# Kernel optimization log

Hardware: AMD Instinct MI355X
Metric: run time of the kernel (lower is better)

The kernel has to match this reference:

```python
import jax, jax.numpy as jnp
import numpy as np

N, E, D, L = 100000, 600000, 128, 5
BN_EPS = 1e-5


def setup_inputs() -> dict:
    key = jax.random.key(0)
    ks = jax.random.split(key, 12)
    x = jax.random.normal(ks[0], (N, D), dtype=jnp.float32)
    edge_index = jax.random.randint(ks[1], (2, E), 0, N, dtype=jnp.int64)
    edge_attr = jax.random.randint(ks[2], (E, D), 0, 4, dtype=jnp.int32)
    # per-layer GCNConv params
    W = jax.random.normal(ks[3], (L, D, D), dtype=jnp.float32) * 0.05
    b = jax.random.normal(ks[4], (L, D), dtype=jnp.float32) * 0.01
    root = jax.random.normal(ks[5], (L, D), dtype=jnp.float32) * 0.05
    # BatchNorm1d eval-mode params / running stats
    gamma = 1.0 + 0.1 * jax.random.normal(ks[6], (L, D), dtype=jnp.float32)
    beta = 0.1 * jax.random.normal(ks[7], (L, D), dtype=jnp.float32)
    mean = 0.1 * jax.random.normal(ks[8], (L, D), dtype=jnp.float32)
    var = 0.5 + jax.random.uniform(ks[9], (L, D), dtype=jnp.float32)
    return {"x": x, "edge_index": edge_index, "edge_attr": edge_attr,
            "W": W, "b": b, "root": root,
            "gamma": gamma, "beta": beta, "mean": mean, "var": var}


def reference(x, edge_index, edge_attr, W, b, root, gamma, beta, mean, var):
    # edge_attr.long() then identity edge_encoder -> integer values used in float math
    e = edge_attr.astype(x.dtype)                      # [E, D]
    row, col = edge_index[0], edge_index[1]            # source j, target i
    # deg = degree(row) + 1 (same every layer since graph is fixed)
    deg = jax.ops.segment_sum(jnp.ones((E,), x.dtype), row, num_segments=N) + 1.0  # [N]
    dinv = deg ** -0.5
    norm = (dinv[row] * dinv[col])[:, None]            # [E, 1]
    h = x
    for l in range(L):
        hl = h @ W[l].T + b[l]                         # Linear(emb_dim, emb_dim)
        msg = norm * jax.nn.relu(hl[row] + e)          # gather + relu + scale  [E, D]
        agg = jax.ops.segment_sum(msg, col, num_segments=N)  # scatter-add at targets
        h = agg + jax.nn.relu(hl + root[l]) / deg[:, None]   # self-loop term
        # BatchNorm1d (eval mode, running stats)
        h = gamma[l] * (h - mean[l]) / jnp.sqrt(var[l] + BN_EPS) + beta[l]
        if l < L - 1:
            h = jax.nn.relu(h)                         # dropout is identity in eval
    return h  # JK='last'
```

## Files before the change

kernel.cpp:

```cpp
#include <hip/hip_runtime.h>
#include <cstdint>
#include <cstddef>

#define DF 128
#define NL 5
#define BN_EPS 1e-5f

typedef short bf16x8 __attribute__((ext_vector_type(8)));
typedef float f32x4 __attribute__((ext_vector_type(4)));

typedef __attribute__((address_space(3))) uint32_t lds_u32;
typedef __attribute__((address_space(1))) uint32_t glb_u32;

__device__ __forceinline__ void gload16(const void* g, void* l) {
#if __has_builtin(__builtin_amdgcn_global_load_lds)
  __builtin_amdgcn_global_load_lds((const glb_u32*)g, (lds_u32*)l, 16, 0, 0);
#else
  *(uint4*)l = *(const uint4*)g;
#endif
}

__device__ __forceinline__ ushort f2b(float f) {
  union { float f; uint32_t u; } v; v.f = f;
  uint32_t u = v.u + 0x7fffu + ((v.u >> 16) & 1u);
  return (ushort)(u >> 16);
}
__device__ __forceinline__ float b2f(uint32_t lo16) {
  union { uint32_t u; float f; } v; v.u = lo16 << 16;
  return v.f;
}
__device__ __forceinline__ uint32_t pk2(float a, float b) {
  return (uint32_t)f2b(a) | ((uint32_t)f2b(b) << 16);
}


__global__ void k_deg2(const int* __restrict__ row, const int* __restrict__ col,
                       int* __restrict__ degi, int* __restrict__ indeg, int E) {
  int i = blockIdx.x * blockDim.x + threadIdx.x;
  if (i < E) {
    atomicAdd(&degi[row[i]], 1);
    atomicAdd(&indeg[col[i]], 1);
  }
}

__global__ void k_dinv(const int* __restrict__ degi, float* __restrict__ dinv, int N) {
  int i = blockIdx.x * blockDim.x + threadIdx.x;
  if (i < N) dinv[i] = 1.0f / sqrtf((float)(degi[i] + 1));
}

__global__ void k_start(const int* __restrict__ indeg, int* __restrict__ start,
                        int* __restrict__ cursor, int* __restrict__ counter, int N) {
  int i = blockIdx.x * blockDim.x + threadIdx.x;
  if (i < N) {
    int s = atomicAdd(counter, indeg[i]);
    start[i] = s;
    cursor[i] = s;
  }
}

__global__ void k_fillpack(const int* __restrict__ row, const int* __restrict__ col,
                           const float* __restrict__ dinv, int* __restrict__ cursor,
                           int* __restrict__ srcS, float* __restrict__ nrmS,
                           const int* __restrict__ ea, uint32_t* __restrict__ epS, int E) {
  int tid = blockIdx.x * blockDim.x + threadIdx.x;
  int e = tid >> 3, t = tid & 7;
  if (e >= E) return;
  int pos;
  if (t == 0) {
    int r = row[e], c = col[e];
    pos = atomicAdd(&cursor[c], 1);
    srcS[pos] = r;
    nrmS[pos] = dinv[r] * dinv[c];
  }
  pos = __shfl(pos, 0, 8);
  const int4* p = ((const int4*)ea) + (size_t)e * 32 + t * 4;
  uint32_t w = 0;
  #pragma unroll
  for (int q = 0; q < 4; ++q) {
    int4 a = p[q];
    w |= ((uint32_t)(a.x & 3)) << (8 * q);
    w |= ((uint32_t)(a.y & 3)) << (8 * q + 2);
    w |= ((uint32_t)(a.z & 3)) << (8 * q + 4);
    w |= ((uint32_t)(a.w & 3)) << (8 * q + 6);
  }
  epS[(size_t)pos * 8 + t] = w;
}

__global__ void k_params(const float* __restrict__ g, const float* __restrict__ be,
                         const float* __restrict__ mn, const float* __restrict__ vr,
                         float* __restrict__ s, float* __restrict__ t,
                         const float* __restrict__ W, ushort* __restrict__ Wb,
                         int nbn, int nw) {
  int i = blockIdx.x * blockDim.x + threadIdx.x;
  if (i < nw) Wb[i] = f2b(W[i]);
  if (i < nbn) {
    float sc = g[i] / sqrtf(vr[i] + BN_EPS);
    s[i] = sc;
    t[i] = be[i] - mn[i] * sc;
  }
}

template <typename IT, typename AT>
__global__ __launch_bounds__(256) void k_gemm(
    const IT* in, const ushort* __restrict__ Wb,
    const float* __restrict__ bl, const float* __restrict__ rootl,
    const float* __restrict__ sl, const float* __restrict__ tl,
    const float* __restrict__ dinv,
    ushort* __restrict__ hl, AT* accOut, int N)
{
  __shared__ uint4 lA[128 * 16];
  __shared__ uint4 lW[128 * 16];
  const int t = threadIdx.x;
  const int row0 = blockIdx.x * 128;
  const int wv = t >> 6;
  const int l  = t & 63;

  #pragma unroll
  for (int it = 0; it < 8; ++it) {
    int ubase = (it * 4 + wv) * 64;
    int lin = ubase + l;
    int r = lin >> 4, u = lin & 15;
    gload16((const uint4*)Wb + (r << 4) + (u ^ (r & 7)), lA  + 0 == nullptr ? nullptr : (void*)(lW + ubase));
  }

  if constexpr (sizeof(IT) == 2) {
    #pragma unroll
    for (int it = 0; it < 8; ++it) {
      int ubase = (it * 4 + wv) * 64;
      int lin = ubase + l;
      int r = lin >> 4, u = lin & 15;
      int gn = row0 + r;
      int gnc = gn < N ? gn : N - 1;
      gload16((const uint4*)in + (size_t)gnc * 16 + (u ^ (r & 7)), (void*)(lA + ubase));
    }
  } else {
    #pragma unroll
    for (int it = 0; it < 8; ++it) {
      int lin = it * 256 + t;
      int r = lin >> 4, u = lin & 15;
      int gn = row0 + r;
      uint4 pk = make_uint4(0u, 0u, 0u, 0u);
      if (gn < N) {
        const float4* p = (const float4*)((const float*)in + (size_t)gn * DF + u * 8);
        float4 f0 = p[0], f1 = p[1];
        pk.x = pk2(f0.x, f0.y); pk.y = pk2(f0.z, f0.w);
        pk.z = pk2(f1.x, f1.y); pk.w = pk2(f1.z, f1.w);
      }
      lA[(r << 4) | (u ^ (r & 7))] = pk;
    }
  }
  __syncthreads();

  const int lr = l & 15;
  const int lk = l >> 4;

  f32x4 acc[2][8];
  #pragma unroll
  for (int rt = 0; rt < 2; ++rt)
    #pragma unroll
    for (int ct = 0; ct < 8; ++ct) acc[rt][ct] = (f32x4){0.f, 0.f, 0.f, 0.f};

  #pragma unroll
  for (int ks = 0; ks < 4; ++ks) {
    const int kofs = ks * 4 + lk;
    bf16x8 af[2], wf[8];
    #pragma unroll
    for (int rt = 0; rt < 2; ++rt) {
      int r = wv * 32 + rt * 16 + lr;
      af[rt] = *reinterpret_cast<const bf16x8*>(&lA[(r << 4) | (kofs ^ (r & 7))]);
    }
    #pragma unroll
    for (int ct = 0; ct < 8; ++ct) {
      int r = ct * 16 + lr;
      wf[ct] = *reinterpret_cast<const bf16x8*>(&lW[(r << 4) | (kofs ^ (r & 7))]);
    }
    #pragma unroll
    for (int rt = 0; rt < 2; ++rt)
      #pragma unroll
      for (int ct = 0; ct < 8; ++ct)
        acc[rt][ct] = __builtin_amdgcn_mfma_f32_16x16x32_bf16(af[rt], wf[ct], acc[rt][ct], 0, 0, 0);
  }

  float bb[8], rr[8], ss[8], tt[8];
  #pragma unroll
  for (int ct = 0; ct < 8; ++ct) {
    int c = ct * 16 + lr;
    bb[ct] = bl[c]; rr[ct] = rootl[c]; ss[ct] = sl[c]; tt[ct] = tl[c];
  }

  #pragma unroll
  for (int rt = 0; rt < 2; ++rt) {
    #pragma unroll
    for (int rg = 0; rg < 4; ++rg) {
      int gn = row0 + wv * 32 + rt * 16 + lk * 4 + rg;
      if (gn >= N) continue;
      float di = dinv[gn];
      float invdeg = di * di;
      #pragma unroll
      for (int ct = 0; ct < 8; ++ct) {
        int c = ct * 16 + lr;
        float o = acc[rt][ct][rg] + bb[ct];
        hl[(size_t)gn * DF + c] = f2b(o);
        float se = fmaxf(o + rr[ct], 0.f) * invdeg;
        float av2 = ss[ct] * se + tt[ct];
        if constexpr (sizeof(AT) == 4) accOut[(size_t)gn * DF + c] = av2;
        else                           accOut[(size_t)gn * DF + c] = f2b(av2);
      }
    }
  }
}

template <typename AT, bool RELU>
__global__ __launch_bounds__(256) void k_gather(
    const int* __restrict__ start, const int* __restrict__ indeg,
    const int* __restrict__ srcS, const float* __restrict__ nrmS,
    const uint32_t* __restrict__ epS,
    const uint4* __restrict__ hl4,
    const float* __restrict__ sl,
    AT* acc, int N)
{
  int gw = (blockIdx.x * blockDim.x + threadIdx.x) >> 6;
  int lane = threadIdx.x & 63;
  int s16 = lane & 15;
  int nd = gw * 4 + (lane >> 4);
  if (nd >= N) return;
  int base = start[nd], n = indeg[nd];
  const uint32_t sh = (s16 & 1) * 16;
  const int dw = s16 >> 1;

  float a[8];
  #pragma unroll
  for (int j = 0; j < 8; ++j) a[j] = 0.f;

  for (int c0 = 0; c0 < n; c0 += 16) {
    int m = min(16, n - c0);
    int myIdx = base + c0 + s16;
    int mySrc = (s16 < m) ? srcS[myIdx] : 0;
    float myNrm = (s16 < m) ? nrmS[myIdx] : 0.f;
    #pragma unroll 2
    for (int k = 0; k < m; ++k) {
      int src = __shfl(mySrc, k, 16);
      float nr = __shfl(myNrm, k, 16);
      uint32_t pw = epS[(size_t)(base + c0 + k) * 8 + dw];
      uint4 hw = hl4[(size_t)src * 16 + s16];
      float h, ev;
      h = b2f(hw.x & 0xffffu); ev = (float)((pw >> (sh + 0)) & 3u);  a[0] += nr * fmaxf(h + ev, 0.f);
      h = b2f(hw.x >> 16);     ev = (float)((pw >> (sh + 2)) & 3u);  a[1] += nr * fmaxf(h + ev, 0.f);
      h = b2f(hw.y & 0xffffu); ev = (float)((pw >> (sh + 4)) & 3u);  a[2] += nr * fmaxf(h + ev, 0.f);
      h = b2f(hw.y >> 16);     ev = (float)((pw >> (sh + 6)) & 3u);  a[3] += nr * fmaxf(h + ev, 0.f);
      h = b2f(hw.z & 0xffffu); ev = (float)((pw >> (sh + 8)) & 3u);  a[4] += nr * fmaxf(h + ev, 0.f);
      h = b2f(hw.z >> 16);     ev = (float)((pw >> (sh + 10)) & 3u); a[5] += nr * fmaxf(h + ev, 0.f);
      h = b2f(hw.w & 0xffffu); ev = (float)((pw >> (sh + 12)) & 3u); a[6] += nr * fmaxf(h + ev, 0.f);
      h = b2f(hw.w >> 16);     ev = (float)((pw >> (sh + 14)) & 3u); a[7] += nr * fmaxf(h + ev, 0.f);
    }
  }

  float s8[8];
  ((float4*)s8)[0] = ((const float4*)sl)[s16 * 2];
  ((float4*)s8)[1] = ((const float4*)sl)[s16 * 2 + 1];

  if constexpr (sizeof(AT) == 2) {
    uint4* ap = (uint4*)acc + (size_t)nd * 16 + s16;
    uint4 p = *ap;
    float o[8];
    o[0] = b2f(p.x & 0xffffu) + s8[0] * a[0];
    o[1] = b2f(p.x >> 16)     + s8[1] * a[1];
    o[2] = b2f(p.y & 0xffffu) + s8[2] * a[2];
    o[3] = b2f(p.y >> 16)     + s8[3] * a[3];
    o[4] = b2f(p.z & 0xffffu) + s8[4] * a[4];
    o[5] = b2f(p.z >> 16)     + s8[5] * a[5];
    o[6] = b2f(p.w & 0xffffu) + s8[6] * a[6];
    o[7] = b2f(p.w >> 16)     + s8[7] * a[7];
    if (RELU) {
      #pragma unroll
      for (int j = 0; j < 8; ++j) o[j] = fmaxf(o[j], 0.f);
    }
    p.x = pk2(o[0], o[1]); p.y = pk2(o[2], o[3]);
    p.z = pk2(o[4], o[5]); p.w = pk2(o[6], o[7]);
    *ap = p;
  } else {
    float4* ap = (float4*)acc + (size_t)nd * 32 + s16 * 2;
    float4 p0 = ap[0], p1 = ap[1];
    p0.x += s8[0] * a[0]; p0.y += s8[1] * a[1];
    p0.z += s8[2] * a[2]; p0.w += s8[3] * a[3];
    p1.x += s8[4] * a[4]; p1.y += s8[5] * a[5];
    p1.z += s8[6] * a[6]; p1.w += s8[7] * a[7];
    if (RELU) {
      p0.x = fmaxf(p0.x, 0.f); p0.y = fmaxf(p0.y, 0.f);
      p0.z = fmaxf(p0.z, 0.f); p0.w = fmaxf(p0.w, 0.f);
      p1.x = fmaxf(p1.x, 0.f); p1.y = fmaxf(p1.y, 0.f);
      p1.z = fmaxf(p1.z, 0.f); p1.w = fmaxf(p1.w, 0.f);
    }
    ap[0] = p0; ap[1] = p1;
  }
}

extern "C" void kernel_launch(void* const* d_in, const int* in_sizes, int n_in,
                              void* d_out, int out_size, void* d_ws, size_t ws_size,
                              hipStream_t stream) {
  const float* x     = (const float*)d_in[0];
  const int*   ei    = (const int*)d_in[1];
  const int*   ea    = (const int*)d_in[2];
  const float* W     = (const float*)d_in[3];
  const float* b     = (const float*)d_in[4];
  const float* root  = (const float*)d_in[5];
  const float* gamma = (const float*)d_in[6];
  const float* beta  = (const float*)d_in[7];
  const float* mean  = (const float*)d_in[8];
  const float* var   = (const float*)d_in[9];

  const int N = in_sizes[0] / DF;
  const int E = in_sizes[1] / 2;
  const int* row = ei;
  const int* col = ei + E;

  char* ws = (char*)d_ws;
  size_t off = 0;
  auto alloc = [&](size_t bytes) -> void* {
    void* p = ws + off;
    off = (off + bytes + 255) & ~(size_t)255;
    return p;
  };
  int*      degi   = (int*)alloc((size_t)N * 4);
  int*      indeg  = (int*)alloc((size_t)N * 4);
  int*      counter= (int*)alloc(256);
  size_t    zspan  = (size_t)((char*)ws + off - (char*)degi);
  float*    dinv   = (float*)alloc((size_t)N * 4);
  int*      startA = (int*)alloc((size_t)N * 4);
  int*      cursor = (int*)alloc((size_t)N * 4);
  int*      srcS   = (int*)alloc((size_t)E * 4);
  float*    nrmS   = (float*)alloc((size_t)E * 4);
  uint32_t* epS    = (uint32_t*)alloc((size_t)E * 8 * 4);
  float*    sbuf   = (float*)alloc((size_t)NL * DF * 4);
  float*    tbuf   = (float*)alloc((size_t)NL * DF * 4);
  ushort*   Wb     = (ushort*)alloc((size_t)NL * DF * DF * 2);
  ushort*   hl     = (ushort*)alloc((size_t)N * DF * 2);
  ushort*   accA   = (ushort*)alloc((size_t)N * DF * 2);

  hipMemsetAsync(degi, 0, zspan, stream);

  k_deg2<<<(E + 255) / 256, 256, 0, stream>>>(row, col, degi, indeg, E);
  k_dinv<<<(N + 255) / 256, 256, 0, stream>>>(degi, dinv, N);
  k_start<<<(N + 255) / 256, 256, 0, stream>>>(indeg, startA, cursor, counter, N);
  k_fillpack<<<(E * 8 + 255) / 256, 256, 0, stream>>>(row, col, dinv, cursor,
                                                      srcS, nrmS, ea, epS, E);
  k_params<<<(NL * DF * DF + 255) / 256, 256, 0, stream>>>(
      gamma, beta, mean, var, sbuf, tbuf, W, Wb, NL * DF, NL * DF * DF);

  float* outp = (float*)d_out;
  const int gemmGrid = (N + 127) / 128;
  const int gathGrid = ((N + 3) / 4 * 64 + 255) / 256;

  k_gemm<float, ushort><<<gemmGrid, 256, 0, stream>>>(
      x, Wb, b, root, sbuf, tbuf, dinv, hl, accA, N);
  k_gather<ushort, true><<<gathGrid, 256, 0, stream>>>(
      startA, indeg, srcS, nrmS, epS, (const uint4*)hl, sbuf, accA, N);

  for (int l = 1; l < NL - 1; ++l) {
    k_gemm<ushort, ushort><<<gemmGrid, 256, 0, stream>>>(
        accA, Wb + (size_t)l * DF * DF, b + (size_t)l * DF, root + (size_t)l * DF,
        sbuf + (size_t)l * DF, tbuf + (size_t)l * DF, dinv, hl, accA, N);
    k_gather<ushort, true><<<gathGrid, 256, 0, stream>>>(
        startA, indeg, srcS, nrmS, epS, (const uint4*)hl,
        sbuf + (size_t)l * DF, accA, N);
  }

  {
    const int l = NL - 1;
    k_gemm<ushort, float><<<gemmGrid, 256, 0, stream>>>(
        accA, Wb + (size_t)l * DF * DF, b + (size_t)l * DF, root + (size_t)l * DF,
        sbuf + (size_t)l * DF, tbuf + (size_t)l * DF, dinv, hl, outp, N);
    k_gather<float, false><<<gathGrid, 256, 0, stream>>>(
        startA, indeg, srcS, nrmS, epS, (const uint4*)hl,
        sbuf + (size_t)l * DF, outp, N);
  }
}
```

Baseline: 464.3 us.

## Renumber nodes by in-degree buckets and move self-loop epilogue into gather

```diff
diff --git a/kernel.cpp b/kernel.cpp
--- a/kernel.cpp
+++ b/kernel.cpp
@@ -4,6 +4,7 @@
 
 #define DF 128
 #define NL 5
+#define NB 1024
 #define BN_EPS 1e-5f
 
 typedef short bf16x8 __attribute__((ext_vector_type(8)));
@@ -43,23 +44,58 @@
   }
 }
 
-__global__ void k_dinv(const int* __restrict__ degi, float* __restrict__ dinv, int N) {
-  int i = blockIdx.x * blockDim.x + threadIdx.x;
-  if (i < N) dinv[i] = 1.0f / sqrtf((float)(degi[i] + 1));
-}
-
-__global__ void k_start(const int* __restrict__ indeg, int* __restrict__ start,
-                        int* __restrict__ cursor, int* __restrict__ counter, int N) {
+__global__ void k_dinvhist(const int* __restrict__ degi, const int* __restrict__ indeg,
+                           float* __restrict__ dinv, int* __restrict__ hist, int N) {
   int i = blockIdx.x * blockDim.x + threadIdx.x;
   if (i < N) {
-    int s = atomicAdd(counter, indeg[i]);
-    start[i] = s;
-    cursor[i] = s;
-  }
+    dinv[i] = 1.0f / sqrtf((float)(degi[i] + 1));
+    atomicAdd(&hist[min(indeg[i], NB - 1)], 1);
+  }
+}
+
+__global__ void k_scan(const int* __restrict__ hist,
+                       int* __restrict__ nodeStart, int* __restrict__ edgeStart) {
+  __shared__ int2 sm[NB];
+  int t = threadIdx.x;
+  int c = hist[t];
+  int2 v; v.x = c; v.y = c * t;
+  sm[t] = v;
+  __syncthreads();
+  for (int off = 1; off < NB; off <<= 1) {
+    int2 add; add.x = 0; add.y = 0;
+    if (t >= off) add = sm[t - off];
+    __syncthreads();
+    sm[t].x += add.x; sm[t].y += add.y;
+    __syncthreads();
+  }
+  nodeStart[t] = sm[t].x - c;
+  edgeStart[t] = sm[t].y - c * t;
+}
+
+__global__ void k_assign(const int* __restrict__ indeg, const float* __restrict__ dinv,
+                         const int* __restrict__ nodeStart, const int* __restrict__ edgeStart,
+                         int* __restrict__ binCursor,
+                         int* __restrict__ perm, int* __restrict__ invperm,
+                         int* __restrict__ startP, int* __restrict__ cursorP,
+                         int* __restrict__ degP, float* __restrict__ dinvP, int N) {
+  int nd = blockIdx.x * blockDim.x + threadIdx.x;
+  if (nd >= N) return;
+  int d = indeg[nd];
+  int bin = min(d, NB - 1);
+  int r = atomicAdd(&binCursor[bin], 1);
+  int i = nodeStart[bin] + r;
+  perm[i] = nd;
+  invperm[nd] = i;
+  int st = edgeStart[bin] + r * d;
+  startP[i] = st;
+  cursorP[i] = st;
+  degP[i] = d;
+  dinvP[i] = dinv[nd];
 }
 
 __global__ void k_fillpack(const int* __restrict__ row, const int* __restrict__ col,
-                           const float* __restrict__ dinv, int* __restrict__ cursor,
+                           const float* __restrict__ dinv, const int* __restrict__ invperm,
+                           int* __restrict__ cursorP,
                            int* __restrict__ srcS, float* __restrict__ nrmS,
                            const int* __restrict__ ea, uint32_t* __restrict__ epS, int E) {
   int tid = blockIdx.x * blockDim.x + threadIdx.x;
@@ -68,8 +104,8 @@
   int pos;
   if (t == 0) {
     int r = row[e], c = col[e];
-    pos = atomicAdd(&cursor[c], 1);
-    srcS[pos] = r;
+    pos = atomicAdd(&cursorP[invperm[c]], 1);
+    srcS[pos] = invperm[r];
     nrmS[pos] = dinv[r] * dinv[c];
   }
   pos = __shfl(pos, 0, 8);
@@ -100,13 +136,11 @@
   }
 }
 
-template <typename IT, typename AT>
+template <typename IT>
 __global__ __launch_bounds__(256) void k_gemm(
-    const IT* in, const ushort* __restrict__ Wb,
-    const float* __restrict__ bl, const float* __restrict__ rootl,
-    const float* __restrict__ sl, const float* __restrict__ tl,
-    const float* __restrict__ dinv,
-    ushort* __restrict__ hl, AT* accOut, int N)
+    const IT* __restrict__ in, const int* __restrict__ perm,
+    const ushort* __restrict__ Wb, const float* __restrict__ bl,
+    ushort* __restrict__ hl, int N)
 {
   __shared__ uint4 lA[128 * 16];
   __shared__ uint4 lW[128 * 16];
@@ -120,7 +154,7 @@
     int ubase = (it * 4 + wv) * 64;
     int lin = ubase + l;
     int r = lin >> 4, u = lin & 15;
-    gload16((const uint4*)Wb + (r << 4) + (u ^ (r & 7)), lA  + 0 == nullptr ? nullptr : (void*)(lW + ubase));
+    gload16((const void*)((const uint4*)Wb + (r << 4) + (u ^ (r & 7))), (void*)(lW + ubase));
   }
 
   if constexpr (sizeof(IT) == 2) {
@@ -131,7 +165,8 @@
       int r = lin >> 4, u = lin & 15;
       int gn = row0 + r;
       int gnc = gn < N ? gn : N - 1;
-      gload16((const uint4*)in + (size_t)gnc * 16 + (u ^ (r & 7)), (void*)(lA + ubase));
+      gload16((const void*)((const uint4*)in + (size_t)gnc * 16 + (u ^ (r & 7))),
+              (void*)(lA + ubase));
     }
   } else {
     #pragma unroll
@@ -141,7 +176,8 @@
       int gn = row0 + r;
       uint4 pk = make_uint4(0u, 0u, 0u, 0u);
       if (gn < N) {
-        const float4* p = (const float4*)((const float*)in + (size_t)gn * DF + u * 8);
+        int src = perm[gn];
+        const float4* p = (const float4*)((const float*)in + (size_t)src * DF + u * 8);
         float4 f0 = p[0], f1 = p[1];
         pk.x = pk2(f0.x, f0.y); pk.y = pk2(f0.z, f0.w);
         pk.z = pk2(f1.x, f1.y); pk.w = pk2(f1.z, f1.w);
@@ -181,12 +217,9 @@
         acc[rt][ct] = __builtin_amdgcn_mfma_f32_16x16x32_bf16(af[rt], wf[ct], acc[rt][ct], 0, 0, 0);
   }
 
-  float bb[8], rr[8], ss[8], tt[8];
-  #pragma unroll
-  for (int ct = 0; ct < 8; ++ct) {
-    int c = ct * 16 + lr;
-    bb[ct] = bl[c]; rr[ct] = rootl[c]; ss[ct] = sl[c]; tt[ct] = tl[c];
-  }
+  float bb[8];
+  #pragma unroll
+  for (int ct = 0; ct < 8; ++ct) bb[ct] = bl[ct * 16 + lr];
 
   #pragma unroll
   for (int rt = 0; rt < 2; ++rt) {
@@ -194,37 +227,32 @@
     for (int rg = 0; rg < 4; ++rg) {
       int gn = row0 + wv * 32 + rt * 16 + lk * 4 + rg;
       if (gn >= N) continue;
-      float di = dinv[gn];
-      float invdeg = di * di;
       #pragma unroll
-      for (int ct = 0; ct < 8; ++ct) {
-        int c = ct * 16 + lr;
-        float o = acc[rt][ct][rg] + bb[ct];
-        hl[(size_t)gn * DF + c] = f2b(o);
-        float se = fmaxf(o + rr[ct], 0.f) * invdeg;
-        float av2 = ss[ct] * se + tt[ct];
-        if constexpr (sizeof(AT) == 4) accOut[(size_t)gn * DF + c] = av2;
-        else                           accOut[(size_t)gn * DF + c] = f2b(av2);
-      }
-    }
-  }
-}
-
-template <typename AT, bool RELU>
+      for (int ct = 0; ct < 8; ++ct)
+        hl[(size_t)gn * DF + ct * 16 + lr] = f2b(acc[rt][ct][rg] + bb[ct]);
+    }
+  }
+}
+
+template <typename AT, bool LAST>
 __global__ __launch_bounds__(256) void k_gather(
-    const int* __restrict__ start, const int* __restrict__ indeg,
+    const int* __restrict__ startP, const int* __restrict__ degP,
+    const float* __restrict__ dinvP,
     const int* __restrict__ srcS, const float* __restrict__ nrmS,
     const uint32_t* __restrict__ epS,
     const uint4* __restrict__ hl4,
-    const float* __restrict__ sl,
-    AT* acc, int N)
+    const float* __restrict__ rootl, const float* __restrict__ sl,
+    const float* __restrict__ tl, const int* __restrict__ perm,
+    AT* __restrict__ acc, int N)
 {
   int gw = (blockIdx.x * blockDim.x + threadIdx.x) >> 6;
   int lane = threadIdx.x & 63;
   int s16 = lane & 15;
-  int nd = gw * 4 + (lane >> 4);
-  if (nd >= N) return;
-  int base = start[nd], n = indeg[nd];
+  int i = gw * 4 + (lane >> 4);
+  if (i >= N) return;
+  int base = startP[i], n = degP[i];
+  float di = dinvP[i];
+  float invdeg = di * di;
   const uint32_t sh = (s16 & 1) * 16;
   const int dw = s16 >> 1;
 
@@ -255,43 +283,37 @@
     }
   }
 
-  float s8[8];
-  ((float4*)s8)[0] = ((const float4*)sl)[s16 * 2];
-  ((float4*)s8)[1] = ((const float4*)sl)[s16 * 2 + 1];
-
-  if constexpr (sizeof(AT) == 2) {
-    uint4* ap = (uint4*)acc + (size_t)nd * 16 + s16;
-    uint4 p = *ap;
-    float o[8];
-    o[0] = b2f(p.x & 0xffffu) + s8[0] * a[0];
-    o[1] = b2f(p.x >> 16)     + s8[1] * a[1];
-    o[2] = b2f(p.y & 0xffffu) + s8[2] * a[2];
-    o[3] = b2f(p.y >> 16)     + s8[3] * a[3];
-    o[4] = b2f(p.z & 0xffffu) + s8[4] * a[4];
-    o[5] = b2f(p.z >> 16)     + s8[5] * a[5];
-    o[6] = b2f(p.w & 0xffffu) + s8[6] * a[6];
-    o[7] = b2f(p.w >> 16)     + s8[7] * a[7];
-    if (RELU) {
-      #pragma unroll
-      for (int j = 0; j < 8; ++j) o[j] = fmaxf(o[j], 0.f);
-    }
+  uint4 hwS = hl4[(size_t)i * 16 + s16];
+  float hs[8];
+  hs[0] = b2f(hwS.x & 0xffffu); hs[1] = b2f(hwS.x >> 16);
+  hs[2] = b2f(hwS.y & 0xffffu); hs[3] = b2f(hwS.y >> 16);
+  hs[4] = b2f(hwS.z & 0xffffu); hs[5] = b2f(hwS.z >> 16);
+  hs[6] = b2f(hwS.w & 0xffffu); hs[7] = b2f(hwS.w >> 16);
+
+  float rr[8], ss[8], tt[8];
+  ((float4*)rr)[0] = ((const float4*)rootl)[s16 * 2]; ((float4*)rr)[1] = ((const float4*)rootl)[s16 * 2 + 1];
+  ((float4*)ss)[0] = ((const float4*)sl)[s16 * 2];    ((float4*)ss)[1] = ((const float4*)sl)[s16 * 2 + 1];
+  ((float4*)tt)[0] = ((const float4*)tl)[s16 * 2];    ((float4*)tt)[1] = ((const float4*)tl)[s16 * 2 + 1];
+
+  float o[8];
+  #pragma unroll
+  for (int j = 0; j < 8; ++j) {
+    float self = fmaxf(hs[j] + rr[j], 0.f) * invdeg;
+    o[j] = ss[j] * (self + a[j]) + tt[j];
+  }
+
+  if constexpr (!LAST) {
+    #pragma unroll
+    for (int j = 0; j < 8; ++j) o[j] = fmaxf(o[j], 0.f);
+    uint4 p;
     p.x = pk2(o[0], o[1]); p.y = pk2(o[2], o[3]);
     p.z = pk2(o[4], o[5]); p.w = pk2(o[6], o[7]);
-    *ap = p;
+    ((uint4*)acc)[(size_t)i * 16 + s16] = p;
   } else {
+    int nd = perm[i];
     float4* ap = (float4*)acc + (size_t)nd * 32 + s16 * 2;
-    float4 p0 = ap[0], p1 = ap[1];
-    p0.x += s8[0] * a[0]; p0.y += s8[1] * a[1];
-    p0.z += s8[2] * a[2]; p0.w += s8[3] * a[3];
-    p1.x += s8[4] * a[4]; p1.y += s8[5] * a[5];
-    p1.z += s8[6] * a[6]; p1.w += s8[7] * a[7];
-    if (RELU) {
-      p0.x = fmaxf(p0.x, 0.f); p0.y = fmaxf(p0.y, 0.f);
-      p0.z = fmaxf(p0.z, 0.f); p0.w = fmaxf(p0.w, 0.f);
-      p1.x = fmaxf(p1.x, 0.f); p1.y = fmaxf(p1.y, 0.f);
-      p1.z = fmaxf(p1.z, 0.f); p1.w = fmaxf(p1.w, 0.f);
-    }
-    ap[0] = p0; ap[1] = p1;
+    ap[0] = make_float4(o[0], o[1], o[2], o[3]);
+    ap[1] = make_float4(o[4], o[5], o[6], o[7]);
   }
 }
 
@@ -321,28 +343,38 @@
     off = (off + bytes + 255) & ~(size_t)255;
     return p;
   };
-  int*      degi   = (int*)alloc((size_t)N * 4);
-  int*      indeg  = (int*)alloc((size_t)N * 4);
-  int*      counter= (int*)alloc(256);
-  size_t    zspan  = (size_t)((char*)ws + off - (char*)degi);
-  float*    dinv   = (float*)alloc((size_t)N * 4);
-  int*      startA = (int*)alloc((size_t)N * 4);
-  int*      cursor = (int*)alloc((size_t)N * 4);
-  int*      srcS   = (int*)alloc((size_t)E * 4);
-  float*    nrmS   = (float*)alloc((size_t)E * 4);
-  uint32_t* epS    = (uint32_t*)alloc((size_t)E * 8 * 4);
-  float*    sbuf   = (float*)alloc((size_t)NL * DF * 4);
-  float*    tbuf   = (float*)alloc((size_t)NL * DF * 4);
-  ushort*   Wb     = (ushort*)alloc((size_t)NL * DF * DF * 2);
-  ushort*   hl     = (ushort*)alloc((size_t)N * DF * 2);
-  ushort*   accA   = (ushort*)alloc((size_t)N * DF * 2);
+  int*      degi    = (int*)alloc((size_t)N * 4);
+  int*      indeg   = (int*)alloc((size_t)N * 4);
+  int*      hist    = (int*)alloc((size_t)NB * 4);
+  int*      binCur  = (int*)alloc((size_t)NB * 4);
+  size_t    zspan   = (size_t)((char*)ws + off - (char*)degi);
+  float*    dinv    = (float*)alloc((size_t)N * 4);
+  int*      nodeSt  = (int*)alloc((size_t)NB * 4);
+  int*      edgeSt  = (int*)alloc((size_t)NB * 4);
+  int*      perm    = (int*)alloc((size_t)N * 4);
+  int*      invperm = (int*)alloc((size_t)N * 4);
+  int*      startP  = (int*)alloc((size_t)N * 4);
+  int*      cursorP = (int*)alloc((size_t)N * 4);
+  int*      degP    = (int*)alloc((size_t)N * 4);
+  float*    dinvP   = (float*)alloc((size_t)N * 4);
+  int*      srcS    = (int*)alloc((size_t)E * 4);
+  float*    nrmS    = (float*)alloc((size_t)E * 4);
+  uint32_t* epS     = (uint32_t*)alloc((size_t)E * 8 * 4);
+  float*    sbuf    = (float*)alloc((size_t)NL * DF * 4);
+  float*    tbuf    = (float*)alloc((size_t)NL * DF * 4);
+  ushort*   Wb      = (ushort*)alloc((size_t)NL * DF * DF * 2);
+  ushort*   hl      = (ushort*)alloc((size_t)N * DF * 2);
+  ushort*   accP    = (ushort*)alloc((size_t)N * DF * 2);
 
   hipMemsetAsync(degi, 0, zspan, stream);
 
   k_deg2<<<(E + 255) / 256, 256, 0, stream>>>(row, col, degi, indeg, E);
-  k_dinv<<<(N + 255) / 256, 256, 0, stream>>>(degi, dinv, N);
-  k_start<<<(N + 255) / 256, 256, 0, stream>>>(indeg, startA, cursor, counter, N);
-  k_fillpack<<<(E * 8 + 255) / 256, 256, 0, stream>>>(row, col, dinv, cursor,
+  k_dinvhist<<<(N + 255) / 256, 256, 0, stream>>>(degi, indeg, dinv, hist, N);
+  k_scan<<<1, NB, 0, stream>>>(hist, nodeSt, edgeSt);
+  k_assign<<<(N + 255) / 256, 256, 0, stream>>>(indeg, dinv, nodeSt, edgeSt, binCur,
+                                                perm, invperm, startP, cursorP,
+                                                degP, dinvP, N);
+  k_fillpack<<<(E * 8 + 255) / 256, 256, 0, stream>>>(row, col, dinv, invperm, cursorP,
                                                       srcS, nrmS, ea, epS, E);
   k_params<<<(NL * DF * DF + 255) / 256, 256, 0, stream>>>(
       gamma, beta, mean, var, sbuf, tbuf, W, Wb, NL * DF, NL * DF * DF);
@@ -351,27 +383,27 @@
   const int gemmGrid = (N + 127) / 128;
   const int gathGrid = ((N + 3) / 4 * 64 + 255) / 256;
 
-  k_gemm<float, ushort><<<gemmGrid, 256, 0, stream>>>(
-      x, Wb, b, root, sbuf, tbuf, dinv, hl, accA, N);
-  k_gather<ushort, true><<<gathGrid, 256, 0, stream>>>(
-      startA, indeg, srcS, nrmS, epS, (const uint4*)hl, sbuf, accA, N);
+  k_gemm<float><<<gemmGrid, 256, 0, stream>>>(x, perm, Wb, b, hl, N);
+  k_gather<ushort, false><<<gathGrid, 256, 0, stream>>>(
+      startP, degP, dinvP, srcS, nrmS, epS, (const uint4*)hl,
+      root, sbuf, tbuf, perm, accP, N);
 
   for (int l = 1; l < NL - 1; ++l) {
-    k_gemm<ushort, ushort><<<gemmGrid, 256, 0, stream>>>(
-        accA, Wb + (size_t)l * DF * DF, b + (size_t)l * DF, root + (size_t)l * DF,
-        sbuf + (size_t)l * DF, tbuf + (size_t)l * DF, dinv, hl, accA, N);
-    k_gather<ushort, true><<<gathGrid, 256, 0, stream>>>(
-        startA, indeg, srcS, nrmS, epS, (const uint4*)hl,
-        sbuf + (size_t)l * DF, accA, N);
+    k_gemm<ushort><<<gemmGrid, 256, 0, stream>>>(
+        accP, nullptr, Wb + (size_t)l * DF * DF, b + (size_t)l * DF, hl, N);
+    k_gather<ushort, false><<<gathGrid, 256, 0, stream>>>(
+        startP, degP, dinvP, srcS, nrmS, epS, (const uint4*)hl,
+        root + (size_t)l * DF, sbuf + (size_t)l * DF, tbuf + (size_t)l * DF,
+        perm, accP, N);
   }
 
   {
     const int l = NL - 1;
-    k_gemm<ushort, float><<<gemmGrid, 256, 0, stream>>>(
-        accA, Wb + (size_t)l * DF * DF, b + (size_t)l * DF, root + (size_t)l * DF,
-        sbuf + (size_t)l * DF, tbuf + (size_t)l * DF, dinv, hl, outp, N);
-    k_gather<float, false><<<gathGrid, 256, 0, stream>>>(
-        startA, indeg, srcS, nrmS, epS, (const uint4*)hl,
-        sbuf + (size_t)l * DF, outp, N);
-  }
-}
+    k_gemm<ushort><<<gemmGrid, 256, 0, stream>>>(
+        accP, nullptr, Wb + (size_t)l * DF * DF, b + (size_t)l * DF, hl, N);
+    k_gather<float, true><<<gathGrid, 256, 0, stream>>>(
+        startP, degP, dinvP, srcS, nrmS, epS, (const uint4*)hl,
+        root + (size_t)l * DF, sbuf + (size_t)l * DF, tbuf + (size_t)l * DF,
+        perm, outp, N);
+  }
+}
```

New measurement: 1.155 ms. 149% more time.
